# Kernel optimization log

Measured on AMD Instinct MI355X. Metric: run time of the kernel, lower is better.

Reference implementation:

```python
import jax, jax.numpy as jnp
import numpy as np

N = 100000   # nodes
E = 1600000  # edges (avg degree 16)
B = 64       # graphs
EPS_MSG = 1e-7   # GENConv message eps
EPS_BN = 1e-5    # BatchNorm eps


def _bn(h, g, b):
    # BatchNorm1d over node dimension (training-mode statistics)
    mu = h.mean(axis=0)
    var = h.var(axis=0)
    return (h - mu) * jax.lax.rsqrt(var + EPS_BN) * g + b


def _genconv(x, src, dst, w1, b1, g1, be1, w2, b2):
    # GENConv: msg = relu(x_j) + eps; softmax aggregation (t=1); residual; 2-layer MLP
    msg = jax.nn.relu(x[src]) + EPS_MSG                      # [E, F]
    mmax = jax.ops.segment_max(msg, dst, num_segments=N)     # [N, F]
    mmax = jnp.where(jnp.isneginf(mmax), 0.0, mmax)          # isolated nodes
    ex = jnp.exp(msg - mmax[dst])                            # [E, F]
    denom = jax.ops.segment_sum(ex, dst, num_segments=N)     # [N, F]
    alpha = ex / (denom[dst] + 1e-16)                        # per-channel softmax
    agg = jax.ops.segment_sum(msg * alpha, dst, num_segments=N)
    out = agg + x                                            # root residual
    h = jax.nn.relu(_bn(out @ w1 + b1, g1, be1))
    return h @ w2 + b2


def setup_inputs() -> dict:
    key = jax.random.key(0)
    ks = jax.random.split(key, 8)
    x = jax.random.normal(ks[0], (N, 6), dtype=jnp.float32)
    edge_index = jax.random.randint(ks[1], (2, E), 0, N, dtype=jnp.int32)
    batch = jnp.sort(jax.random.randint(ks[2], (N,), 0, B, dtype=jnp.int32))
    s = 0.1
    return {
        "x": x, "edge_index": edge_index, "batch": batch,
        "cin_w1": jax.random.normal(ks[3], (6, 12)) * s,
        "cin_b1": jnp.zeros((12,)), "cin_g1": jnp.ones((12,)), "cin_be1": jnp.zeros((12,)),
        "cin_w2": jax.random.normal(ks[4], (12, 64)) * s, "cin_b2": jnp.zeros((64,)),
        "L_w1": jax.random.normal(ks[5], (3, 64, 128)) * s, "L_b1": jnp.zeros((3, 128)),
        "L_g1": jnp.ones((3, 128)), "L_be1": jnp.zeros((3, 128)),
        "L_w2": jax.random.normal(ks[6], (3, 128, 64)) * s, "L_b2": jnp.zeros((3, 64)),
        "mlp_w1": jax.random.normal(ks[7], (64, 64)) * s, "mlp_b1": jnp.zeros((64,)),
        "mlp_w2": jax.random.normal(jax.random.fold_in(key, 9), (64, 80)) * s,
        "mlp_b2": jnp.zeros((80,)),
    }


def reference(x, edge_index, batch, cin_w1, cin_b1, cin_g1, cin_be1, cin_w2, cin_b2,
              L_w1, L_b1, L_g1, L_be1, L_w2, L_b2, mlp_w1, mlp_b1, mlp_w2, mlp_b2):
    src, dst = edge_index[0], edge_index[1]
    h = jax.nn.relu(_genconv(x, src, dst, cin_w1, cin_b1, cin_g1, cin_be1, cin_w2, cin_b2))
    for i in range(3):  # DeepGCNLayer res+ (norm=None, dropout identity in eval)
        delta = _genconv(jax.nn.relu(h), src, dst, L_w1[i], L_b1[i], L_g1[i], L_be1[i], L_w2[i], L_b2[i])
        h = h + delta
    g = jax.ops.segment_max(h, batch, num_segments=B)  # global_max_pool -> [B, 64]
    g = jnp.where(jnp.isneginf(g), 0.0, g)
    return jax.nn.relu(g @ mlp_w1 + mlp_b1) @ mlp_w2 + mlp_b2  # [B, 80]
```

## Files before the change

kernel.cpp:

```cpp
#include <hip/hip_runtime.h>

#define NN 100000
#define EE 1600000
#define BB 64
#define NSCAN 98
#define AG6 1024
#define AG64 640
#define NTILE 1563
#define POOL_BLK 512
#define POOL_WAVES (POOL_BLK * 4)
#define HCLS 8

typedef float f32x4 __attribute__((ext_vector_type(4)));
typedef short short8 __attribute__((ext_vector_type(8)));

__device__ __forceinline__ unsigned fmap(float f) {
  unsigned u = __float_as_uint(f);
  return (u & 0x80000000u) ? ~u : (u | 0x80000000u);
}
__device__ __forceinline__ float funmap(unsigned m) {
  unsigned u = (m & 0x80000000u) ? (m ^ 0x80000000u) : ~m;
  return __uint_as_float(u);
}
__device__ __forceinline__ unsigned short f2b(float f) {
  unsigned u = __float_as_uint(f);
  unsigned r = (u + 0x7FFFu + ((u >> 16) & 1u)) >> 16;
  return (unsigned short)r;
}
__device__ __forceinline__ float b2f(unsigned short s) {
  return __uint_as_float(((unsigned)s) << 16);
}

__global__ void k_hist8(const int* __restrict__ dst, int* __restrict__ counts8,
                        int* __restrict__ rank) {
  int i = blockIdx.x * blockDim.x + threadIdx.x;
  int c = blockIdx.x & (HCLS - 1);
  if (i < EE) rank[i] = atomicAdd(&counts8[c * NN + dst[i]], 1);
}

__global__ void k_off8(int* __restrict__ counts8, int* __restrict__ counts) {
  int n = blockIdx.x * blockDim.x + threadIdx.x;
  if (n >= NN) return;
  int t = 0;
#pragma unroll
  for (int c = 0; c < HCLS; ++c) {
    int v = counts8[c * NN + n];
    counts8[c * NN + n] = t;
    t += v;
  }
  counts[n] = t;
}

__global__ void k_scan1(const int* __restrict__ counts, int* __restrict__ rowptr,
                        int* __restrict__ partials) {
  __shared__ int buf[1024];
  int i = blockIdx.x * 1024 + threadIdx.x;
  int v = (i < NN) ? counts[i] : 0;
  buf[threadIdx.x] = v;
  __syncthreads();
  for (int off = 1; off < 1024; off <<= 1) {
    int t = (threadIdx.x >= off) ? buf[threadIdx.x - off] : 0;
    __syncthreads();
    buf[threadIdx.x] += t;
    __syncthreads();
  }
  int incl = buf[threadIdx.x];
  if (i < NN) rowptr[i] = incl - v;
  if (threadIdx.x == 1023) partials[blockIdx.x] = incl;
}

__global__ void k_scan2(const int* __restrict__ partials, int* __restrict__ poffs,
                        unsigned* __restrict__ gmax) {
  __shared__ int buf[128];
  int t = threadIdx.x;
  int v = (t < NSCAN) ? partials[t] : 0;
  buf[t] = v;
  __syncthreads();
  for (int off = 1; off < 128; off <<= 1) {
    int u = (t >= off) ? buf[t - off] : 0;
    __syncthreads();
    buf[t] += u;
    __syncthreads();
  }
  poffs[t] = buf[t] - v;
  for (int i = t; i < BB * 64; i += 128) gmax[i] = 0x007FFFFFu;
}

__global__ void k_scan3(int* __restrict__ rowptr, const int* __restrict__ poffs) {
  int i = blockIdx.x * 1024 + threadIdx.x;
  if (i < NN) rowptr[i] += poffs[blockIdx.x];
  if (i == 0) rowptr[NN] = EE;
}

__global__ __launch_bounds__(256) void k_place(const int* __restrict__ src,
                                               const int* __restrict__ dst,
                                               const int* __restrict__ rank,
                                               const int* __restrict__ rowptr,
                                               const int* __restrict__ counts8,
                                               int* __restrict__ adjsrc) {
  int i = blockIdx.x * blockDim.x + threadIdx.x;
  if (i < EE) {
    int c = (i >> 8) & (HCLS - 1);
    int d = dst[i];
    adjsrc[rowptr[d] + counts8[c * NN + d] + rank[i]] = src[i];
  }
}

__global__ __launch_bounds__(256) void k_agg0(const float* __restrict__ xin,
                                              const int* __restrict__ rowptr,
                                              const int* __restrict__ adjsrc,
                                              float* __restrict__ out) {
  int w = __builtin_amdgcn_readfirstlane(threadIdx.x >> 6);
  int lane = threadIdx.x & 63;
  int wid = blockIdx.x * 4 + w;
  if (wid >= NN) return;
  int s = rowptr[wid], e = rowptr[wid + 1];
  bool act = lane < 6;
  float den = 0.f, num = 0.f;
  int i = s;
  for (; i + 3 < e; i += 4) {
    int n0 = adjsrc[i], n1 = adjsrc[i + 1], n2 = adjsrc[i + 2], n3 = adjsrc[i + 3];
    float v0 = act ? xin[(size_t)n0 * 6 + lane] : 0.f;
    float v1 = act ? xin[(size_t)n1 * 6 + lane] : 0.f;
    float v2 = act ? xin[(size_t)n2 * 6 + lane] : 0.f;
    float v3 = act ? xin[(size_t)n3 * 6 + lane] : 0.f;
    float m0 = fminf(fmaxf(v0, 0.f) + 1e-7f, 80.f);
    float m1 = fminf(fmaxf(v1, 0.f) + 1e-7f, 80.f);
    float m2 = fminf(fmaxf(v2, 0.f) + 1e-7f, 80.f);
    float m3 = fminf(fmaxf(v3, 0.f) + 1e-7f, 80.f);
    float e0 = __expf(m0), e1 = __expf(m1), e2 = __expf(m2), e3 = __expf(m3);
    den += (e0 + e1) + (e2 + e3);
    num += (m0 * e0 + m1 * e1) + (m2 * e2 + m3 * e3);
  }
  for (; i < e; ++i) {
    int n0 = adjsrc[i];
    float v0 = act ? xin[(size_t)n0 * 6 + lane] : 0.f;
    float m0 = fminf(fmaxf(v0, 0.f) + 1e-7f, 80.f);
    float e0 = __expf(m0);
    den += e0;
    num += m0 * e0;
  }
  if (act) {
    float xr = xin[(size_t)wid * 6 + lane];
    out[(size_t)wid * 6 + lane] = num / (den + 1e-16f) + xr;
  }
}

__global__ __launch_bounds__(256) void k_aggb(const unsigned short* __restrict__ xb,
                                              const float* __restrict__ h,
                                              const int* __restrict__ rowptr,
                                              const int* __restrict__ adjsrc,
                                              float* __restrict__ out) {
  int w = __builtin_amdgcn_readfirstlane(threadIdx.x >> 6);
  int lane = threadIdx.x & 63;
  int wid = blockIdx.x * 4 + w;
  if (wid >= NN) return;
  int s = rowptr[wid], e = rowptr[wid + 1];
  float den = 0.f, num = 0.f;
  int i = s;
  for (; i + 3 < e; i += 4) {
    int n0 = adjsrc[i], n1 = adjsrc[i + 1], n2 = adjsrc[i + 2], n3 = adjsrc[i + 3];
    float v0 = b2f(xb[(size_t)n0 * 64 + lane]);
    float v1 = b2f(xb[(size_t)n1 * 64 + lane]);
    float v2 = b2f(xb[(size_t)n2 * 64 + lane]);
    float v3 = b2f(xb[(size_t)n3 * 64 + lane]);
    float m0 = fminf(v0 + 1e-7f, 80.f);
    float m1 = fminf(v1 + 1e-7f, 80.f);
    float m2 = fminf(v2 + 1e-7f, 80.f);
    float m3 = fminf(v3 + 1e-7f, 80.f);
    float e0 = __expf(m0), e1 = __expf(m1), e2 = __expf(m2), e3 = __expf(m3);
    den += (e0 + e1) + (e2 + e3);
    num += (m0 * e0 + m1 * e1) + (m2 * e2 + m3 * e3);
  }
  for (; i < e; ++i) {
    int n0 = adjsrc[i];
    float v0 = b2f(xb[(size_t)n0 * 64 + lane]);
    float m0 = fminf(v0 + 1e-7f, 80.f);
    float e0 = __expf(m0);
    den += e0;
    num += m0 * e0;
  }
  float res = fmaxf(h[(size_t)wid * 64 + lane], 0.f);
  out[(size_t)wid * 64 + lane] = num / (den + 1e-16f) + res;
}

__global__ __launch_bounds__(256) void k_ata6(const float* __restrict__ A,
                                              float* __restrict__ part) {
  constexpr int F = 6;
  int lane = threadIdx.x & 63;
  int w = __builtin_amdgcn_readfirstlane(threadIdx.x >> 6);
  bool act = lane < F;
  float Sloc[F];
#pragma unroll
  for (int c = 0; c < F; ++c) Sloc[c] = 0.f;
  float csloc = 0.f;
  int NW = gridDim.x * 4;
  for (int node = blockIdx.x * 4 + w; node < NN; node += NW) {
    float a = act ? A[(size_t)node * F + lane] : 0.f;
    csloc += a;
#pragma unroll
    for (int c = 0; c < F; ++c) {
      float ac = __shfl(a, c, 64);
      Sloc[c] += ac * a;
    }
  }
  __shared__ float ls[F * F + F];
  for (int idx = threadIdx.x; idx < F * F + F; idx += 256) ls[idx] = 0.f;
  __syncthreads();
  if (act) {
#pragma unroll
    for (int c = 0; c < F; ++c) atomicAdd(&ls[c * F + lane], Sloc[c]);
    atomicAdd(&ls[F * F + lane], csloc);
  }
  __syncthreads();
  float* dstp = part + (size_t)blockIdx.x * (F * F + F);
  for (int idx = threadIdx.x; idx < F * F + F; idx += 256) dstp[idx] = ls[idx];
}

__global__ __launch_bounds__(256) void k_ata64(const float* __restrict__ A,
                                               float* __restrict__ part) {
  __shared__ float lA[64 * 64];
  __shared__ float lcs[64];
  int tid = threadIdx.x;
  int tx = tid & 15, ty = tid >> 4;
  float acc[4][4];
#pragma unroll
  for (int i = 0; i < 4; ++i)
#pragma unroll
    for (int j = 0; j < 4; ++j) acc[i][j] = 0.f;
  float cs0 = 0.f, cs1 = 0.f, cs2 = 0.f, cs3 = 0.f;
  if (tid < 64) lcs[tid] = 0.f;
  const float4* A4 = (const float4*)A;
  for (int tile = blockIdx.x; tile < NTILE; tile += gridDim.x) {
    int nbase = tile * 64;
    __syncthreads();
#pragma unroll
    for (int k = 0; k < 4; ++k) {
      int node = ty + k * 16;
      int gn = nbase + node;
      float4 v = (gn < NN) ? A4[(size_t)gn * 16 + tx]
                           : make_float4(0.f, 0.f, 0.f, 0.f);
      *(float4*)&lA[node * 64 + tx * 4] = v;
      cs0 += v.x; cs1 += v.y; cs2 += v.z; cs3 += v.w;
    }
    __syncthreads();
#pragma unroll 4
    for (int node = 0; node < 64; ++node) {
      float4 rv = *(const float4*)&lA[node * 64 + ty * 4];
      float4 cv = *(const float4*)&lA[node * 64 + tx * 4];
      acc[0][0] += rv.x * cv.x; acc[0][1] += rv.x * cv.y;
      acc[0][2] += rv.x * cv.z; acc[0][3] += rv.x * cv.w;
      acc[1][0] += rv.y * cv.x; acc[1][1] += rv.y * cv.y;
      acc[1][2] += rv.y * cv.z; acc[1][3] += rv.y * cv.w;
      acc[2][0] += rv.z * cv.x; acc[2][1] += rv.z * cv.y;
      acc[2][2] += rv.z * cv.z; acc[2][3] += rv.z * cv.w;
      acc[3][0] += rv.w * cv.x; acc[3][1] += rv.w * cv.y;
      acc[3][2] += rv.w * cv.z; acc[3][3] += rv.w * cv.w;
    }
  }
  __syncthreads();
  atomicAdd(&lcs[tx * 4 + 0], cs0);
  atomicAdd(&lcs[tx * 4 + 1], cs1);
  atomicAdd(&lcs[tx * 4 + 2], cs2);
  atomicAdd(&lcs[tx * 4 + 3], cs3);
  float* dstp = part + (size_t)blockIdx.x * 4160;
#pragma unroll
  for (int i = 0; i < 4; ++i)
#pragma unroll
    for (int j = 0; j < 4; ++j)
      dstp[(ty * 4 + i) * 64 + tx * 4 + j] = acc[i][j];
  __syncthreads();
  if (tid < 64) dstp[4096 + tid] = lcs[tid];
}

__global__ void k_redB(const float* __restrict__ part, float* __restrict__ out,
                       int stride, int ngrid) {
  __shared__ float buf[256];
  int i = blockIdx.x;
  float s = 0.f;
  for (int g = threadIdx.x; g < ngrid; g += 256) s += part[(size_t)g * stride + i];
  buf[threadIdx.x] = s;
  __syncthreads();
  for (int off = 128; off; off >>= 1) {
    if (threadIdx.x < off) buf[threadIdx.x] += buf[threadIdx.x + off];
    __syncthreads();
  }
  if (threadIdx.x == 0) out[i] = buf[0];
}

template<int FIN, int FMID>
__global__ void k_bnprep(const float* __restrict__ S, const float* __restrict__ cs,
                         const float* __restrict__ Wm, const float* __restrict__ bm,
                         const float* __restrict__ gamma, const float* __restrict__ beta,
                         float* __restrict__ ab) {
  int j = blockIdx.x;
  int lane = threadIdx.x;
  bool act = (FIN == 64) || (lane < FIN);
  float wj = act ? Wm[lane * FMID + j] : 0.f;
  float mb = act ? cs[lane] * (1.f / NN) : 0.f;
  float t = mb * wj;
#pragma unroll
  for (int off = 32; off; off >>= 1) t += __shfl_xor(t, off, 64);
  float mulin = t;
  float acc = 0.f;
  for (int c = 0; c < FIN; ++c) {
    float sv = act ? S[c * FIN + lane] : 0.f;
    float p = sv * wj;
#pragma unroll
    for (int off = 32; off; off >>= 1) p += __shfl_xor(p, off, 64);
    acc += p * __shfl(wj, c, 64);
  }
  if (lane == 0) {
    float var = acc * (1.f / NN) - mulin * mulin;
    float rstd = rsqrtf(fmaxf(var, 0.f) + 1e-5f);
    float sc = rstd * gamma[j];
    ab[j] = sc;
    ab[FMID + j] = beta[j] - mulin * sc;
  }
}

template<int FIN, int FMID, int FOUT>
__global__ __launch_bounds__(256) void k_layer(const float* __restrict__ A,
                                               const float* __restrict__ Wm,
                                               const float* __restrict__ ab,
                                               const float* __restrict__ W2,
                                               const float* __restrict__ b2,
                                               float* __restrict__ H,
                                               unsigned short* __restrict__ XB) {
  constexpr int SM = FMID + 1;
  constexpr int MW = FMID / 4;
  constexpr int OW = FOUT / 4;
  __shared__ float lA[FIN * 65];
  __shared__ float lH_sep[64 * SM];
  int tid = threadIdx.x;
  int lane = tid & 63;
  int w = __builtin_amdgcn_readfirstlane(tid >> 6);
  int nbase = blockIdx.x * 64;
  for (int e = tid; e < 64 * FIN; e += 256) {
    int node = e / FIN, c = e - node * FIN;
    int gn = nbase + node;
    lA[c * 65 + node] = (gn < NN) ? A[(size_t)gn * FIN + c] : 0.f;
  }
  __syncthreads();
  float acc[MW];
#pragma unroll
  for (int j = 0; j < MW; ++j) acc[j] = 0.f;
#pragma unroll 4
  for (int c = 0; c < FIN; ++c) {
    float a = lA[c * 65 + lane];
#pragma unroll
    for (int j = 0; j < MW; ++j) acc[j] += a * Wm[c * FMID + w * MW + j];
  }
#pragma unroll
  for (int j = 0; j < MW; ++j) {
    float sc = ab[w * MW + j];
    float sh = ab[FMID + w * MW + j];
    lH_sep[lane * SM + w * MW + j] = fmaxf(acc[j] * sc + sh, 0.f);
  }
  __syncthreads();
  float acc2[OW];
#pragma unroll
  for (int j = 0; j < OW; ++j) acc2[j] = b2[w * OW + j];
#pragma unroll 4
  for (int c = 0; c < FMID; ++c) {
    float hv = lH_sep[lane * SM + c];
#pragma unroll
    for (int j = 0; j < OW; ++j) acc2[j] += hv * W2[c * FOUT + w * OW + j];
  }
  int node = nbase + lane;
  if (node < NN) {
    size_t base = (size_t)node * FOUT + w * OW;
#pragma unroll
    for (int j = 0; j < OW; ++j) {
      float hn = fmaxf(acc2[j], 0.f);
      H[base + j] = hn;
      XB[base + j] = f2b(hn);
    }
  }
}

__global__ void k_packW(const float* __restrict__ L_w1, const float* __restrict__ L_w2,
                        short* __restrict__ wmf, short* __restrict__ w2f) {
  int idx = blockIdx.x * 256 + threadIdx.x;
  if (idx >= 3 * 16384) return;
  int layer = idx / 16384;
  int r = idx - layer * 16384;
  bool isW2 = r >= 8192;
  int e = isW2 ? r - 8192 : r;
  int j = e & 7, lane = (e >> 3) & 63, t = e >> 9;
  int kgrp = lane >> 4, nlow = lane & 15;
  if (!isW2) {
    int nt = t >> 1, kc = t & 1;
    int k = kc * 32 + 8 * kgrp + j, n = nt * 16 + nlow;
    wmf[(size_t)layer * 8192 + e] = (short)f2b(L_w1[(size_t)layer * 64 * 128 + k * 128 + n]);
  } else {
    int nt = t >> 2, kc = t & 3;
    int k = kc * 32 + 8 * kgrp + j, n = nt * 16 + nlow;
    w2f[(size_t)layer * 8192 + e] = (short)f2b(L_w2[(size_t)layer * 128 * 64 + k * 64 + n]);
  }
}

__global__ __launch_bounds__(256) void k_layerM(const float* __restrict__ A,
                                                const short* __restrict__ Wmf,
                                                const float* __restrict__ ab,
                                                const short* __restrict__ W2f,
                                                const float* __restrict__ b2,
                                                float* __restrict__ H,
                                                unsigned short* __restrict__ XB) {
  __shared__ short lFrag[8192];
  __shared__ float ls_ab[256];
  int tid = threadIdx.x;
  int lane = tid & 63;
  int w = tid >> 6;
  int nbase = blockIdx.x * 64;
  ls_ab[tid] = ab[tid];
#pragma unroll
  for (int it = 0; it < 2; ++it) {
    int e = tid + 256 * it;
    int ln = e & 63;
    int m = (e >> 6) & 3;
    int kc = e >> 8;
    int row = nbase + 16 * m + (ln & 15);
    int k0 = 32 * kc + 8 * (ln >> 4);
    short8 v;
    if (row < NN) {
      const float* ap = &A[(size_t)row * 64 + k0];
#pragma unroll
      for (int j = 0; j < 8; ++j) v[j] = (short)f2b(ap[j]);
    } else {
#pragma unroll
      for (int j = 0; j < 8; ++j) v[j] = 0;
    }
    *(short8*)&lFrag[((kc * 4 + m) * 64 + ln) * 8] = v;
  }
  __syncthreads();
  f32x4 acc[4][2];
#pragma unroll
  for (int m = 0; m < 4; ++m) {
    acc[m][0] = (f32x4){0.f, 0.f, 0.f, 0.f};
    acc[m][1] = (f32x4){0.f, 0.f, 0.f, 0.f};
  }
  short8 bf[2][2];
#pragma unroll
  for (int kc = 0; kc < 2; ++kc)
#pragma unroll
    for (int t = 0; t < 2; ++t) {
      int nt = 2 * w + t;
      bf[kc][t] = *(const short8*)&Wmf[(((nt * 2 + kc) * 64) + lane) * 8];
    }
#pragma unroll
  for (int kc = 0; kc < 2; ++kc)
#pragma unroll
    for (int m = 0; m < 4; ++m) {
      short8 af = *(short8*)&lFrag[((kc * 4 + m) * 64 + lane) * 8];
      acc[m][0] = __builtin_amdgcn_mfma_f32_16x16x32_bf16(af, bf[kc][0], acc[m][0], 0, 0, 0);
      acc[m][1] = __builtin_amdgcn_mfma_f32_16x16x32_bf16(af, bf[kc][1], acc[m][1], 0, 0, 0);
    }
  __syncthreads();
#pragma unroll
  for (int t = 0; t < 2; ++t) {
    int nt = 2 * w + t;
    int ch = 16 * nt + (lane & 15);
    float sc = ls_ab[ch];
    float sh = ls_ab[128 + ch];
    int kc2 = ch >> 5;
    int lgrp = (ch & 31) >> 3;
    int j2 = ch & 7;
#pragma unroll
    for (int m = 0; m < 4; ++m) {
#pragma unroll
      for (int r = 0; r < 4; ++r) {
        float mv = fmaxf(acc[m][t][r] * sc + sh, 0.f);
        int lp = lgrp * 16 + (lane >> 4) * 4 + r;
        lFrag[((kc2 * 4 + m) * 64 + lp) * 8 + j2] = (short)f2b(mv);
      }
    }
  }
  __syncthreads();
  float bias = b2[16 * w + (lane & 15)];
  f32x4 acc2[4];
#pragma unroll
  for (int m = 0; m < 4; ++m) acc2[m] = (f32x4){bias, bias, bias, bias};
#pragma unroll
  for (int kc = 0; kc < 4; ++kc) {
    short8 b2fr = *(const short8*)&W2f[(((w * 4 + kc) * 64) + lane) * 8];
#pragma unroll
    for (int m = 0; m < 4; ++m) {
      short8 af = *(short8*)&lFrag[((kc * 4 + m) * 64 + lane) * 8];
      acc2[m] = __builtin_amdgcn_mfma_f32_16x16x32_bf16(af, b2fr, acc2[m], 0, 0, 0);
    }
  }
  int colch = 16 * w + (lane & 15);
#pragma unroll
  for (int m = 0; m < 4; ++m) {
#pragma unroll
    for (int r = 0; r < 4; ++r) {
      int node = nbase + 16 * m + (lane >> 4) * 4 + r;
      if (node < NN) {
        size_t idx = (size_t)node * 64 + colch;
        float hn = H[idx] + acc2[m][r];
        H[idx] = hn;
        XB[idx] = f2b(fmaxf(hn, 0.f));
      }
    }
  }
}

__global__ __launch_bounds__(256) void k_pool(const float* __restrict__ h,
                                              const int* __restrict__ batch,
                                              unsigned* __restrict__ gmax) {
  int wgid = blockIdx.x * 4 + (threadIdx.x >> 6);
  int lane = threadIdx.x & 63;
  const int per = (NN + POOL_WAVES - 1) / POOL_WAVES;
  int n0 = wgid * per;
  int n1 = min(n0 + per, NN);
  if (n0 >= NN) return;
  int g = batch[n0];
  float m = -INFINITY;
  for (int node = n0; node < n1; ++node) {
    int b = batch[node];
    if (b != g) {
      atomicMax(&gmax[(g << 6) + lane], fmap(m));
      m = -INFINITY;
      g = b;
    }
    m = fmaxf(m, h[(size_t)node * 64 + lane]);
  }
  atomicMax(&gmax[(g << 6) + lane], fmap(m));
}

__global__ void k_final(const unsigned* __restrict__ gmax, const float* __restrict__ w1,
                        const float* __restrict__ b1, const float* __restrict__ w2,
                        const float* __restrict__ b2, float* __restrict__ out) {
  int b = blockIdx.x;
  __shared__ float g[64], hid[64];
  int t = threadIdx.x;
  if (t < 64) {
    float v = funmap(gmax[b * 64 + t]);
    if (v == -INFINITY) v = 0.f;
    g[t] = v;
  }
  __syncthreads();
  if (t < 64) {
    float acc = b1[t];
    for (int c = 0; c < 64; ++c) acc += g[c] * w1[c * 64 + t];
    hid[t] = fmaxf(acc, 0.f);
  }
  __syncthreads();
  if (t < 80) {
    float acc = b2[t];
    for (int c = 0; c < 64; ++c) acc += hid[c] * w2[c * 80 + t];
    out[b * 80 + t] = acc;
  }
}

extern "C" void kernel_launch(void* const* d_in, const int* in_sizes, int n_in,
                              void* d_out, int out_size, void* d_ws, size_t ws_size,
                              hipStream_t stream) {
  const float* x       = (const float*)d_in[0];
  const int*   ei      = (const int*)d_in[1];
  const int*   batch   = (const int*)d_in[2];
  const float* cin_w1  = (const float*)d_in[3];
  const float* cin_b1  = (const float*)d_in[4];
  const float* cin_g1  = (const float*)d_in[5];
  const float* cin_be1 = (const float*)d_in[6];
  const float* cin_w2  = (const float*)d_in[7];
  const float* cin_b2  = (const float*)d_in[8];
  const float* L_w1    = (const float*)d_in[9];
  const float* L_b1    = (const float*)d_in[10];
  const float* L_g1    = (const float*)d_in[11];
  const float* L_be1   = (const float*)d_in[12];
  const float* L_w2    = (const float*)d_in[13];
  const float* L_b2    = (const float*)d_in[14];
  const float* mlp_w1  = (const float*)d_in[15];
  const float* mlp_b1  = (const float*)d_in[16];
  const float* mlp_w2  = (const float*)d_in[17];
  const float* mlp_b2  = (const float*)d_in[18];

  char* ws = (char*)d_ws;
  size_t off = 0;
  auto alloc = [&](size_t bytes) -> void* {
    void* p = ws + off;
    off = (off + bytes + 255) & ~(size_t)255;
    return p;
  };
  float*          A       = (float*)alloc((size_t)NN * 64 * 4);
  float*          h       = (float*)alloc((size_t)NN * 64 * 4);
  unsigned short* xb      = (unsigned short*)alloc((size_t)NN * 64 * 2);
  int*            rowptr  = (int*)alloc((size_t)(NN + 1) * 4);
  int*            counts  = (int*)alloc((size_t)NN * 4);
  int*            counts8 = (int*)alloc((size_t)HCLS * NN * 4);
  int*            rank    = (int*)alloc((size_t)EE * 4);
  int*            adjsrc  = (int*)alloc((size_t)EE * 4);
  int*            partial = (int*)alloc(NSCAN * 4);
  int*            poffs   = (int*)alloc(128 * 4);
  short*          wmf     = (short*)alloc((size_t)3 * 8192 * 2);
  short*          w2f     = (short*)alloc((size_t)3 * 8192 * 2);
  float*          part    = (float*)alloc((size_t)AG6 * 4160 * 4);
  float*          Sfin    = (float*)alloc((size_t)4 * 4160 * 4);
  float*          ab      = (float*)alloc((size_t)4 * 256 * 4);
  unsigned*       gmax    = (unsigned*)alloc((size_t)BB * 64 * 4);
  (void)ws_size; (void)in_sizes; (void)n_in; (void)out_size;

  const int* srcp = ei;
  const int* dstp = ei + EE;

  hipMemsetAsync(counts8, 0, (size_t)HCLS * NN * 4, stream);
  k_hist8<<<(EE + 255) / 256, 256, 0, stream>>>(dstp, counts8, rank);
  k_packW<<<192, 256, 0, stream>>>(L_w1, L_w2, wmf, w2f);
  k_off8<<<(NN + 255) / 256, 256, 0, stream>>>(counts8, counts);
  k_scan1<<<NSCAN, 1024, 0, stream>>>(counts, rowptr, partial);
  k_scan2<<<1, 128, 0, stream>>>(partial, poffs, gmax);
  k_scan3<<<NSCAN, 1024, 0, stream>>>(rowptr, poffs);
  k_place<<<(EE + 255) / 256, 256, 0, stream>>>(srcp, dstp, rank, rowptr, counts8, adjsrc);

  const int NB64 = (NN + 63) / 64;

  {
    float* S = Sfin;
    float* cs = S + 6 * 6;
    float* ab0 = ab;
    k_agg0<<<NN / 4, 256, 0, stream>>>(x, rowptr, adjsrc, A);
    k_ata6<<<AG6, 256, 0, stream>>>(A, part);
    k_redB<<<42, 256, 0, stream>>>(part, S, 42, AG6);
    k_bnprep<6, 12><<<12, 64, 0, stream>>>(S, cs, cin_w1, cin_b1, cin_g1, cin_be1, ab0);
    k_layer<6, 12, 64><<<NB64, 256, 0, stream>>>(A, cin_w1, ab0, cin_w2, cin_b2, h, xb);
  }

  for (int i = 0; i < 3; ++i) {
    float* S = Sfin + (size_t)(i + 1) * 4160;
    float* cs = S + 64 * 64;
    float* abi = ab + (size_t)(i + 1) * 256;
    k_aggb<<<NN / 4, 256, 0, stream>>>(xb, h, rowptr, adjsrc, A);
    k_ata64<<<AG64, 256, 0, stream>>>(A, part);
    k_redB<<<4160, 256, 0, stream>>>(part, S, 4160, AG64);
    k_bnprep<64, 128><<<128, 64, 0, stream>>>(S, cs, L_w1 + (size_t)i * 64 * 128,
                                              L_b1 + i * 128, L_g1 + i * 128,
                                              L_be1 + i * 128, abi);
    k_layerM<<<NB64, 256, 0, stream>>>(A, wmf + (size_t)i * 8192, abi,
                                       w2f + (size_t)i * 8192, L_b2 + i * 64, h, xb);
  }

  k_pool<<<POOL_BLK, 256, 0, stream>>>(h, batch, gmax);
  k_final<<<BB, 128, 0, stream>>>(gmax, mlp_w1, mlp_b1, mlp_w2, mlp_b2, (float*)d_out);
}
```

Baseline: 583.1 us.

## Vectorize bf16 neighbor gathers in 64-channel aggregation with 16-byte loads

The per-node softmax aggregation kernel now has each wavefront process 16 edges per iteration. Each lane loads 8 bf16 channels of one neighbor as a uint4 instead of one 2-byte element per lane. Partial sums over the 8 edge slots are combined with cross-lane shuffles, and one lane group writes the results with float4 stores. The goal is fewer, wider memory transactions on the random gather, at the cost of shuffle reductions, more registers, and wasted lanes on low-degree nodes.

Measured after the change: 609.0 us. 4.4% more time.

```diff
diff --git a/kernel.cpp b/kernel.cpp
--- a/kernel.cpp
+++ b/kernel.cpp
@@ -146,42 +146,70 @@
   }
 }
 
-__global__ __launch_bounds__(256) void k_aggb(const unsigned short* __restrict__ xb,
+__global__ __launch_bounds__(256) void k_aggb(const uint4* __restrict__ xb4,
                                               const float* __restrict__ h,
                                               const int* __restrict__ rowptr,
                                               const int* __restrict__ adjsrc,
                                               float* __restrict__ out) {
   int w = __builtin_amdgcn_readfirstlane(threadIdx.x >> 6);
-  int lane = threadIdx.x & 63;
   int wid = blockIdx.x * 4 + w;
   if (wid >= NN) return;
+  int lane = threadIdx.x & 63;
+  int eslot = lane >> 3;
+  int cgrp = lane & 7;
   int s = rowptr[wid], e = rowptr[wid + 1];
-  float den = 0.f, num = 0.f;
-  int i = s;
-  for (; i + 3 < e; i += 4) {
-    int n0 = adjsrc[i], n1 = adjsrc[i + 1], n2 = adjsrc[i + 2], n3 = adjsrc[i + 3];
-    float v0 = b2f(xb[(size_t)n0 * 64 + lane]);
-    float v1 = b2f(xb[(size_t)n1 * 64 + lane]);
-    float v2 = b2f(xb[(size_t)n2 * 64 + lane]);
-    float v3 = b2f(xb[(size_t)n3 * 64 + lane]);
-    float m0 = fminf(v0 + 1e-7f, 80.f);
-    float m1 = fminf(v1 + 1e-7f, 80.f);
-    float m2 = fminf(v2 + 1e-7f, 80.f);
-    float m3 = fminf(v3 + 1e-7f, 80.f);
-    float e0 = __expf(m0), e1 = __expf(m1), e2 = __expf(m2), e3 = __expf(m3);
-    den += (e0 + e1) + (e2 + e3);
-    num += (m0 * e0 + m1 * e1) + (m2 * e2 + m3 * e3);
-  }
-  for (; i < e; ++i) {
-    int n0 = adjsrc[i];
-    float v0 = b2f(xb[(size_t)n0 * 64 + lane]);
-    float m0 = fminf(v0 + 1e-7f, 80.f);
-    float e0 = __expf(m0);
-    den += e0;
-    num += m0 * e0;
-  }
-  float res = fmaxf(h[(size_t)wid * 64 + lane], 0.f);
-  out[(size_t)wid * 64 + lane] = num / (den + 1e-16f) + res;
+  float den[8], num[8];
+#pragma unroll
+  for (int j = 0; j < 8; ++j) { den[j] = 0.f; num[j] = 0.f; }
+  for (int base = s; base < e; base += 16) {
+    int ei0 = base + eslot;
+    int ei1 = base + 8 + eslot;
+    bool v0 = ei0 < e, v1 = ei1 < e;
+    int n0 = adjsrc[v0 ? ei0 : e - 1];
+    int n1 = adjsrc[v1 ? ei1 : e - 1];
+    uint4 u0 = xb4[(size_t)n0 * 8 + cgrp];
+    uint4 u1 = xb4[(size_t)n1 * 8 + cgrp];
+    unsigned uu0[4] = {u0.x, u0.y, u0.z, u0.w};
+    unsigned uu1[4] = {u1.x, u1.y, u1.z, u1.w};
+#pragma unroll
+    for (int p = 0; p < 4; ++p) {
+      float alo = __uint_as_float(uu0[p] << 16);
+      float ahi = __uint_as_float(uu0[p] & 0xffff0000u);
+      float mlo = fminf(alo + 1e-7f, 80.f);
+      float mhi = fminf(ahi + 1e-7f, 80.f);
+      float elo = v0 ? __expf(mlo) : 0.f;
+      float ehi = v0 ? __expf(mhi) : 0.f;
+      den[2 * p] += elo;     num[2 * p] += mlo * elo;
+      den[2 * p + 1] += ehi; num[2 * p + 1] += mhi * ehi;
+      float blo = __uint_as_float(uu1[p] << 16);
+      float bhi = __uint_as_float(uu1[p] & 0xffff0000u);
+      float nlo = fminf(blo + 1e-7f, 80.f);
+      float nhi = fminf(bhi + 1e-7f, 80.f);
+      float flo = v1 ? __expf(nlo) : 0.f;
+      float fhi = v1 ? __expf(nhi) : 0.f;
+      den[2 * p] += flo;     num[2 * p] += nlo * flo;
+      den[2 * p + 1] += fhi; num[2 * p + 1] += nhi * fhi;
+    }
+  }
+#pragma unroll
+  for (int j = 0; j < 8; ++j) {
+    den[j] += __shfl_xor(den[j], 8, 64);
+    num[j] += __shfl_xor(num[j], 8, 64);
+    den[j] += __shfl_xor(den[j], 16, 64);
+    num[j] += __shfl_xor(num[j], 16, 64);
+    den[j] += __shfl_xor(den[j], 32, 64);
+    num[j] += __shfl_xor(num[j], 32, 64);
+  }
+  if (eslot == 0) {
+    float o[8];
+#pragma unroll
+    for (int j = 0; j < 8; ++j) {
+      float res = fmaxf(h[(size_t)wid * 64 + 8 * cgrp + j], 0.f);
+      o[j] = num[j] / (den[j] + 1e-16f) + res;
+    }
+    *(float4*)&out[(size_t)wid * 64 + 8 * cgrp] = make_float4(o[0], o[1], o[2], o[3]);
+    *(float4*)&out[(size_t)wid * 64 + 8 * cgrp + 4] = make_float4(o[4], o[5], o[6], o[7]);
+  }
 }
 
 __global__ __launch_bounds__(256) void k_ata6(const float* __restrict__ A,
@@ -631,7 +659,7 @@
     float* S = Sfin + (size_t)(i + 1) * 4160;
     float* cs = S + 64 * 64;
     float* abi = ab + (size_t)(i + 1) * 256;
-    k_aggb<<<NN / 4, 256, 0, stream>>>(xb, h, rowptr, adjsrc, A);
+    k_aggb<<<NN / 4, 256, 0, stream>>>((const uint4*)xb, h, rowptr, adjsrc, A);
     k_ata64<<<AG64, 256, 0, stream>>>(A, part);
     k_redB<<<4160, 256, 0, stream>>>(part, S, 4160, AG64);
     k_bnprep<64, 128><<<128, 64, 0, stream>>>(S, cs, L_w1 + (size_t)i * 64 * 128,
```
